# Performance work log

Measured on AMD Instinct MI355X. Metric: run time of the kernel, lower is better.

The kernel has to match this reference:

```python
import jax, jax.numpy as jnp
import numpy as np

G = 2048   # geneNum
E = 512    # emb_len
B = 16     # batch


def setup_inputs() -> dict:
    key = jax.random.key(0)
    ks = jax.random.split(key, 12)
    xav = 1.0 / np.sqrt(2.0)  # xavier gain used in reset_parameters

    def xavier(k, shape, gain):
        fan_in, fan_out = shape[1], shape[0]
        a = gain * np.sqrt(6.0 / (fan_in + fan_out))
        return jax.random.uniform(k, shape, jnp.float32, -a, a)

    return {
        "datax": jax.random.randint(ks[0], (B, G), 0, 5),
        "embMat": jax.random.normal(ks[1], (G, E), jnp.float32),      # frozen embedding table
        "Wq": xavier(ks[2], (E, E), xav),
        "Wk": xavier(ks[3], (E, E), xav),
        "k1": jax.random.normal(ks[4], (G, G), jnp.float32),
        "k2": jax.random.normal(ks[5], (G, G), jnp.float32),
        "k3": jax.random.normal(ks[6], (1,), jnp.float32),
        "shortestPath": jax.random.randint(ks[7], (G, G), 1, 8).astype(jnp.float32),
        "centralityMat": jax.random.uniform(ks[8], (G, G), jnp.float32),
        "padding": (jax.random.uniform(ks[9], (G, G)) > 0.1).astype(jnp.float32),
        "fc1_w": xavier(ks[10], (G, G), xav),
        "fc1_b": jnp.zeros((G,), jnp.float32),
        "fcCox_w": xavier(ks[11], (1, G), xav),
    }


def reference(datax, embMat, Wq, Wk, k1, k2, k3, shortestPath,
              centralityMat, padding, fc1_w, fc1_b, fcCox_w):
    # In torch, originalx aliases x, so the in-place binarization makes the
    # embedding indices binary (0/1).
    xbin = (datax != 0).astype(jnp.int32)          # [B, G]
    originalx = xbin.astype(jnp.float32)           # [B, G]
    x = embMat[xbin]                               # [B, G, E] (rows 0/1 of table)

    q = jnp.einsum('bge,fe->bgf', x, Wq)           # Linear no-bias: x @ Wq.T
    k = jnp.einsum('bge,fe->bgf', x, Wk)

    attn_weights = jnp.einsum('bge,bhe->bgh', q, k)  # [B, G, G]
    lrelu = lambda t: jax.nn.leaky_relu(t, 0.01)
    bias = (lrelu(k1) * shortestPath
            + lrelu(k2) * centralityMat
            + lrelu(k3) * padding)                 # [G, G]
    attn_weights = attn_weights + bias
    attn_weights_origin = attn_weights

    aw = jax.nn.softmax(attn_weights, axis=-1)     # [B, G, G]
    v = (datax != 0).astype(jnp.float32)           # binary values, [B, G]
    attn = jnp.einsum('bgh,bh->bg', aw, v)         # bmm with [B,G,1] + squeeze
    # Dropout(p=0.2) -> identity (eval / deterministic baseline)
    attn = originalx + attn
    attn = attn @ fc1_w.T + fc1_b                  # fc1
    output = attn @ fcCox_w.T                      # [B, 1]
    return output.reshape(-1), attn_weights_origin
```

## Files before the change

### kernel.cpp

```cpp
#include <hip/hip_runtime.h>
#include <stdint.h>

#define GN 2048
#define EN 512
#define BN 16

typedef unsigned int nt_u32x4 __attribute__((ext_vector_type(4)));
typedef float        nt_f32x4 __attribute__((ext_vector_type(4)));

__device__ __forceinline__ float bf2f(unsigned short u) {
    return __uint_as_float(((unsigned int)u) << 16);
}
__device__ __forceinline__ unsigned short f2bf(float f) {
    unsigned int u = __float_as_uint(f);
    u += 0x7fffu + ((u >> 16) & 1u);
    return (unsigned short)(u >> 16);
}
__device__ __forceinline__ float lrelu(float v) { return v > 0.f ? v : 0.01f * v; }

union U16x8 { uint4 v; nt_u32x4 e; unsigned short s[8]; };

template<bool ISBF>
__device__ __forceinline__ float ldf(const void* p, size_t i) {
    if (ISBF) return bf2f(((const unsigned short*)p)[i]);
    return ((const float*)p)[i];
}

template<bool ISBF>
__device__ __forceinline__ void ld8(const void* p, size_t off, float* v) {
    if (ISBF) {
        U16x8 u; u.v = *(const uint4*)((const unsigned short*)p + off);
        #pragma unroll
        for (int i = 0; i < 8; i++) v[i] = bf2f(u.s[i]);
    } else {
        const float* q = (const float*)p + off;
        const float4 a = *(const float4*)q;
        const float4 b = *(const float4*)(q + 4);
        v[0]=a.x; v[1]=a.y; v[2]=a.z; v[3]=a.w;
        v[4]=b.x; v[5]=b.y; v[6]=b.z; v[7]=b.w;
    }
}

template<bool ISBF>
__device__ __forceinline__ void st8(void* p, size_t off, const float* v) {
    if (ISBF) {
        U16x8 u;
        #pragma unroll
        for (int i = 0; i < 8; i++) u.s[i] = f2bf(v[i]);
        *(uint4*)((unsigned short*)p + off) = u.v;
    } else {
        float* q = (float*)p + off;
        *(float4*)q       = make_float4(v[0], v[1], v[2], v[3]);
        *(float4*)(q + 4) = make_float4(v[4], v[5], v[6], v[7]);
    }
}

__global__ void sniff_k(const unsigned int* __restrict__ emb, int* __restrict__ flag) {
    const int t = threadIdx.x;
    const unsigned int w = emb[t];
    const int e = (w >> 7) & 0xFF;
    const int ok = (e >= 108 && e <= 134) ? 1 : 0;
    const unsigned long long m = __ballot(ok);
    if (t == 0) flag[0] = (__popcll(m) >= 40) ? 1 : 0;
}

template<bool ISBF>
__device__ __forceinline__ void setup_body(
    const int* __restrict__ datax, const void* emb, const void* Wq, const void* Wk,
    const void* fc1w, const void* fcCox,
    unsigned char* __restrict__ xpackT, float* __restrict__ qk,
    float* __restrict__ partials)
{
    const int blk = blockIdx.x;
    const int t = threadIdx.x;

    if (blk < 16) {
        const int b = blk;
        unsigned int byte = 0;
        const int base = b * GN + t * 8;
        #pragma unroll
        for (int i = 0; i < 8; i++)
            byte |= (datax[base + i] != 0 ? 1u : 0u) << i;
        xpackT[t * 16 + b] = (unsigned char)byte;
    } else if (blk < 272) {
        const int iw = (blk - 16) * 4 + (t >> 6);
        const int lane = t & 63;
        const void* W = (iw < 512) ? Wq : Wk;
        const int f = iw & 511;
        float w8[8], e0[8], e1[8];
        ld8<ISBF>(W, (size_t)f * EN + lane * 8, w8);
        ld8<ISBF>(emb, (size_t)lane * 8, e0);
        ld8<ISBF>(emb, (size_t)EN + lane * 8, e1);
        float d0 = 0.f, d1 = 0.f;
        #pragma unroll
        for (int i = 0; i < 8; i++) { d0 += w8[i] * e0[i]; d1 += w8[i] * e1[i]; }
        for (int o = 32; o >= 1; o >>= 1) {
            d0 += __shfl_xor(d0, o);
            d1 += __shfl_xor(d1, o);
        }
        if (lane == 0) {
            const int base = (iw < 512) ? 0 : 1024;
            qk[base + f] = d0;
            qk[base + 512 + f] = d1;
        }
    } else {
        const int pb = blk - 272;
        float acc[8] = {0.f,0.f,0.f,0.f,0.f,0.f,0.f,0.f};
        for (int r = 0; r < 16; r++) {
            const int g = pb * 16 + r;
            const float c = ldf<ISBF>(fcCox, g);
            float w8[8];
            ld8<ISBF>(fc1w, (size_t)g * GN + t * 8, w8);
            #pragma unroll
            for (int i = 0; i < 8; i++) acc[i] += c * w8[i];
        }
        float* q = partials + (size_t)pb * GN + t * 8;
        *(float4*)q       = make_float4(acc[0], acc[1], acc[2], acc[3]);
        *(float4*)(q + 4) = make_float4(acc[4], acc[5], acc[6], acc[7]);
    }
}

__global__ __launch_bounds__(256) void setup_k(
    const int* datax, const void* emb, const void* Wq, const void* Wk,
    const void* fc1w, const void* fcCox,
    unsigned char* xpackT, float* qk, float* partials, const int* flag)
{
    if (flag[0]) setup_body<true>(datax, emb, Wq, Wk, fc1w, fcCox, xpackT, qk, partials);
    else         setup_body<false>(datax, emb, Wq, Wk, fc1w, fcCox, xpackT, qk, partials);
}

template<bool ISBF>
__device__ __forceinline__ void pre2_body(
    const float* __restrict__ qk, const void* fc1b, const void* fcCox,
    const float* __restrict__ partials,
    float* __restrict__ sv, float* __restrict__ cptr, float* __restrict__ weff)
{
    const int t = threadIdx.x;
    if (blockIdx.x > 0) {
        const int c = (blockIdx.x - 1) * 256 + t;
        float acc = 0.f;
        for (int r = 0; r < 128; r++)
            acc += partials[(size_t)r * GN + c];
        weff[c] = acc;
        return;
    }
    float a[5] = {0.f, 0.f, 0.f, 0.f, 0.f};
    for (int e = t; e < EN; e += 256) {
        float q0 = qk[e], q1 = qk[EN + e];
        float K0 = qk[2 * EN + e], K1 = qk[3 * EN + e];
        a[0] += q0 * K0; a[1] += q0 * K1; a[2] += q1 * K0; a[3] += q1 * K1;
    }
    for (int gg = t; gg < GN; gg += 256)
        a[4] += ldf<ISBF>(fc1b, gg) * ldf<ISBF>(fcCox, gg);
    for (int o = 32; o >= 1; o >>= 1)
        #pragma unroll
        for (int j = 0; j < 5; j++) a[j] += __shfl_xor(a[j], o);
    __shared__ float red[4][5];
    int wid = t >> 6, lane = t & 63;
    if (lane == 0)
        for (int j = 0; j < 5; j++) red[wid][j] = a[j];
    __syncthreads();
    if (t == 0) {
        for (int j = 0; j < 4; j++)
            sv[j] = red[0][j] + red[1][j] + red[2][j] + red[3][j];
        cptr[0] = red[0][4] + red[1][4] + red[2][4] + red[3][4];
    }
}

__global__ __launch_bounds__(256) void pre2_k(
    const float* qk, const void* fc1b, const void* fcCox, const float* partials,
    float* sv, float* cptr, float* weff, const int* flag)
{
    if (flag[0]) pre2_body<true>(qk, fc1b, fcCox, partials, sv, cptr, weff);
    else         pre2_body<false>(qk, fc1b, fcCox, partials, sv, cptr, weff);
}

template<bool ISBF>
__device__ __forceinline__ void attn_body(
    const void* k1, const void* k2, const void* k3,
    const void* sp, const void* cen, const void* pad,
    const unsigned char* __restrict__ xpackT, const float* __restrict__ sv,
    float* __restrict__ attn2, void* d_out)
{
    const int g = blockIdx.x;
    const int t = threadIdx.x;
    const int h0 = t << 3;
    const size_t roff = (size_t)g * GN + h0;

    const float lr3 = lrelu(ldf<ISBF>(k3, 0));

    float a1[8], a2[8], vsp[8], vcn[8], vpd[8];
    ld8<ISBF>(k1, roff, a1);
    ld8<ISBF>(k2, roff, a2);
    ld8<ISBF>(sp, roff, vsp);
    ld8<ISBF>(cen, roff, vcn);
    ld8<ISBF>(pad, roff, vpd);

    float bias8[8];
    float lmax = -3.4e38f;
    #pragma unroll
    for (int i = 0; i < 8; i++) {
        float b = lrelu(a1[i]) * vsp[i] + lrelu(a2[i]) * vcn[i] + lr3 * vpd[i];
        bias8[i] = b;
        lmax = fmaxf(lmax, b);
    }
    for (int o = 32; o >= 1; o >>= 1) lmax = fmaxf(lmax, __shfl_xor(lmax, o));

    __shared__ float smax[4];
    __shared__ float redT[4];
    __shared__ float red[4][BN];
    const int wid = t >> 6, lane = t & 63;
    if (lane == 0) smax[wid] = lmax;
    __syncthreads();
    const float Mg = fmaxf(fmaxf(smax[0], smax[1]), fmaxf(smax[2], smax[3]));

    float E8[8];
    float Tl = 0.f;
    #pragma unroll
    for (int i = 0; i < 8; i++) { E8[i] = __expf(bias8[i] - Mg); Tl += E8[i]; }

    const uint4 pk = *(const uint4*)(xpackT + (size_t)t * 16);
    const unsigned char* pb = (const unsigned char*)&pk;

    float s1l[BN];
    #pragma unroll
    for (int b = 0; b < BN; b++) {
        const unsigned int mk = pb[b];
        float acc1 = 0.f;
        #pragma unroll
        for (int i = 0; i < 8; i++)
            acc1 += ((mk >> i) & 1u) ? E8[i] : 0.f;
        s1l[b] = acc1;
    }
    for (int o = 32; o >= 1; o >>= 1) {
        Tl += __shfl_xor(Tl, o);
        #pragma unroll
        for (int b = 0; b < BN; b++) s1l[b] += __shfl_xor(s1l[b], o);
    }
    if (lane == 0) {
        redT[wid] = Tl;
        #pragma unroll
        for (int b = 0; b < BN; b++) red[wid][b] = s1l[b];
    }
    __syncthreads();

    const float s00 = sv[0], s01 = sv[1], s10 = sv[2], s11 = sv[3];
    const uint4 gk = *(const uint4*)(xpackT + (size_t)(g >> 3) * 16);
    const unsigned char* gb = (const unsigned char*)&gk;
    const int gbit = g & 7;

    if (t < BN) {
        const int b = t;
        const float Tg = redT[0] + redT[1] + redT[2] + redT[3];
        const float S1 = fmaxf(red[0][b] + red[1][b] + red[2][b] + red[3][b], 1e-30f);
        const float S0 = fmaxf(Tg - S1, 1e-30f);
        const bool on = ((gb[b] >> gbit) & 1u) != 0u;
        const float sa0 = on ? s10 : s00;
        const float sa1 = on ? s11 : s01;
        const float d = (sa0 + __logf(S0)) - (sa1 + __logf(S1));
        const float attnv = 1.f / (1.f + __expf(d));
        attn2[b * GN + g] = (on ? 1.f : 0.f) + attnv;
    }

    if (ISBF) {
        U16x8 p00, p01, p10, p11;
        #pragma unroll
        for (int i = 0; i < 8; i++) {
            p00.s[i] = f2bf(bias8[i] + s00);
            p01.s[i] = f2bf(bias8[i] + s01);
            p10.s[i] = f2bf(bias8[i] + s10);
            p11.s[i] = f2bf(bias8[i] + s11);
        }
        unsigned short* outp = (unsigned short*)d_out + BN + (size_t)g * GN + h0;
        #pragma unroll
        for (int b = 0; b < BN; b++) {
            const unsigned int mk = pb[b];
            const bool on = ((gb[b] >> gbit) & 1u) != 0u;
            U16x8 lo, hi;
            if (on) { lo = p10; hi = p11; } else { lo = p00; hi = p01; }
            U16x8 o;
            #pragma unroll
            for (int i = 0; i < 8; i++)
                o.s[i] = ((mk >> i) & 1u) ? hi.s[i] : lo.s[i];
            __builtin_nontemporal_store(o.e, (nt_u32x4*)(outp + (size_t)b * GN * GN));
        }
    } else {
        float v00[8], v01[8], v10[8], v11[8];
        #pragma unroll
        for (int i = 0; i < 8; i++) {
            v00[i] = bias8[i] + s00;
            v01[i] = bias8[i] + s01;
            v10[i] = bias8[i] + s10;
            v11[i] = bias8[i] + s11;
        }
        float* outp = (float*)d_out + BN + (size_t)g * GN + h0;
        #pragma unroll
        for (int b = 0; b < BN; b++) {
            const unsigned int mk = pb[b];
            const bool on = ((gb[b] >> gbit) & 1u) != 0u;
            float ov[8];
            #pragma unroll
            for (int i = 0; i < 8; i++) {
                const float lo = on ? v10[i] : v00[i];
                const float hi = on ? v11[i] : v01[i];
                ov[i] = ((mk >> i) & 1u) ? hi : lo;
            }
            float* q = outp + (size_t)b * GN * GN;
            nt_f32x4 lo4 = {ov[0], ov[1], ov[2], ov[3]};
            nt_f32x4 hi4 = {ov[4], ov[5], ov[6], ov[7]};
            __builtin_nontemporal_store(lo4, (nt_f32x4*)q);
            __builtin_nontemporal_store(hi4, (nt_f32x4*)(q + 4));
        }
    }
}

__global__ __launch_bounds__(256) void attn_k(
    const void* k1, const void* k2, const void* k3,
    const void* sp, const void* cen, const void* pad,
    const unsigned char* xpackT, const float* sv, float* attn2,
    void* d_out, const int* flag)
{
    if (flag[0]) attn_body<true>(k1, k2, k3, sp, cen, pad, xpackT, sv, attn2, d_out);
    else         attn_body<false>(k1, k2, k3, sp, cen, pad, xpackT, sv, attn2, d_out);
}

template<bool ISBF>
__device__ __forceinline__ void final_body(
    const float* __restrict__ attn2, const float* __restrict__ weff,
    const float* __restrict__ cptr, void* d_out)
{
    const int b = blockIdx.x, t = threadIdx.x;
    const int h0 = t << 3;
    const float4 a0 = *(const float4*)(attn2 + b * GN + h0);
    const float4 a1 = *(const float4*)(attn2 + b * GN + h0 + 4);
    const float4 w0 = *(const float4*)(weff + h0);
    const float4 w1 = *(const float4*)(weff + h0 + 4);
    float acc = a0.x * w0.x + a0.y * w0.y + a0.z * w0.z + a0.w * w0.w
              + a1.x * w1.x + a1.y * w1.y + a1.z * w1.z + a1.w * w1.w;
    for (int o = 32; o >= 1; o >>= 1) acc += __shfl_xor(acc, o);
    __shared__ float red[4];
    const int wid = t >> 6, lane = t & 63;
    if (lane == 0) red[wid] = acc;
    __syncthreads();
    if (t == 0) {
        const float val = cptr[0] + red[0] + red[1] + red[2] + red[3];
        if (ISBF) ((unsigned short*)d_out)[b] = f2bf(val);
        else      ((float*)d_out)[b] = val;
    }
}

__global__ __launch_bounds__(256) void final_k(
    const float* attn2, const float* weff, const float* cptr,
    void* d_out, const int* flag)
{
    if (flag[0]) final_body<true>(attn2, weff, cptr, d_out);
    else         final_body<false>(attn2, weff, cptr, d_out);
}

extern "C" void kernel_launch(void* const* d_in, const int* in_sizes, int n_in,
                              void* d_out, int out_size, void* d_ws, size_t ws_size,
                              hipStream_t stream) {
    const int*  datax = (const int*)d_in[0];
    const void* emb   = d_in[1];
    const void* Wq    = d_in[2];
    const void* Wk    = d_in[3];
    const void* k1    = d_in[4];
    const void* k2    = d_in[5];
    const void* k3    = d_in[6];
    const void* sp    = d_in[7];
    const void* cen   = d_in[8];
    const void* pad   = d_in[9];
    const void* fc1w  = d_in[10];
    const void* fc1b  = d_in[11];
    const void* fcCox = d_in[12];

    float* ws       = (float*)d_ws;
    float* qk       = ws;
    float* sv       = ws + 2048;
    float* cptr     = ws + 2052;
    float* weff     = ws + 2056;
    float* attn2    = ws + 4104;
    float* partials = ws + 36872;
    unsigned char* xpackT = (unsigned char*)(ws + 299016);
    int*   flag     = (int*)(ws + 300040);

    sniff_k<<<1, 64, 0, stream>>>((const unsigned int*)emb, flag);
    setup_k<<<400, 256, 0, stream>>>(datax, emb, Wq, Wk, fc1w, fcCox,
                                     xpackT, qk, partials, flag);
    pre2_k<<<9, 256, 0, stream>>>(qk, fc1b, fcCox, partials, sv, cptr, weff, flag);
    attn_k<<<GN, 256, 0, stream>>>(k1, k2, k3, sp, cen, pad, xpackT, sv, attn2, d_out, flag);
    final_k<<<BN, 256, 0, stream>>>(attn2, weff, cptr, d_out, flag);
}
```

Before: 454.2 us.

## Split attention kernel into bias/softmax pass and batch-wise output writer

The fused attention kernel is split into two kernels. The first computes the bias matrix once, writes it to a workspace buffer and does the softmax reductions. The second reads the bias back and writes the 16 batch slices, with each block covering one batch and 16 rows so writes are contiguous per batch. Nontemporal stores are also replaced with plain stores. This adds a 16 MB bias write and reread, plus an extra launch, in exchange for a different output write pattern. It depends on workspace size and falls back to the old kernel otherwise.

After: 515.4 us. 13.5% more time.

```diff
diff --git a/kernel.cpp b/kernel.cpp
--- a/kernel.cpp
+++ b/kernel.cpp
@@ -4,9 +4,6 @@
 #define GN 2048
 #define EN 512
 #define BN 16
-
-typedef unsigned int nt_u32x4 __attribute__((ext_vector_type(4)));
-typedef float        nt_f32x4 __attribute__((ext_vector_type(4)));
 
 __device__ __forceinline__ float bf2f(unsigned short u) {
     return __uint_as_float(((unsigned int)u) << 16);
@@ -18,7 +15,7 @@
 }
 __device__ __forceinline__ float lrelu(float v) { return v > 0.f ? v : 0.01f * v; }
 
-union U16x8 { uint4 v; nt_u32x4 e; unsigned short s[8]; };
+union U16x8 { uint4 v; unsigned short s[8]; };
 
 template<bool ISBF>
 __device__ __forceinline__ float ldf(const void* p, size_t i) {
@@ -38,20 +35,6 @@
         const float4 b = *(const float4*)(q + 4);
         v[0]=a.x; v[1]=a.y; v[2]=a.z; v[3]=a.w;
         v[4]=b.x; v[5]=b.y; v[6]=b.z; v[7]=b.w;
-    }
-}
-
-template<bool ISBF>
-__device__ __forceinline__ void st8(void* p, size_t off, const float* v) {
-    if (ISBF) {
-        U16x8 u;
-        #pragma unroll
-        for (int i = 0; i < 8; i++) u.s[i] = f2bf(v[i]);
-        *(uint4*)((unsigned short*)p + off) = u.v;
-    } else {
-        float* q = (float*)p + off;
-        *(float4*)q       = make_float4(v[0], v[1], v[2], v[3]);
-        *(float4*)(q + 4) = make_float4(v[4], v[5], v[6], v[7]);
     }
 }
 
@@ -176,6 +159,160 @@
 }
 
 template<bool ISBF>
+__device__ __forceinline__ void attnA_body(
+    const void* k1, const void* k2, const void* k3,
+    const void* sp, const void* cen, const void* pad,
+    const unsigned char* __restrict__ xpackT, const float* __restrict__ sv,
+    float* __restrict__ attn2, float* __restrict__ biasws)
+{
+    const int g = blockIdx.x;
+    const int t = threadIdx.x;
+    const int h0 = t << 3;
+    const size_t roff = (size_t)g * GN + h0;
+
+    const float lr3 = lrelu(ldf<ISBF>(k3, 0));
+
+    float a1[8], a2[8], vsp[8], vcn[8], vpd[8];
+    ld8<ISBF>(k1, roff, a1);
+    ld8<ISBF>(k2, roff, a2);
+    ld8<ISBF>(sp, roff, vsp);
+    ld8<ISBF>(cen, roff, vcn);
+    ld8<ISBF>(pad, roff, vpd);
+
+    float bias8[8];
+    float lmax = -3.4e38f;
+    #pragma unroll
+    for (int i = 0; i < 8; i++) {
+        float b = lrelu(a1[i]) * vsp[i] + lrelu(a2[i]) * vcn[i] + lr3 * vpd[i];
+        bias8[i] = b;
+        lmax = fmaxf(lmax, b);
+    }
+    float* bq = biasws + roff;
+    *(float4*)bq       = make_float4(bias8[0], bias8[1], bias8[2], bias8[3]);
+    *(float4*)(bq + 4) = make_float4(bias8[4], bias8[5], bias8[6], bias8[7]);
+
+    for (int o = 32; o >= 1; o >>= 1) lmax = fmaxf(lmax, __shfl_xor(lmax, o));
+
+    __shared__ float smax[4];
+    __shared__ float redT[4];
+    __shared__ float red[4][BN];
+    const int wid = t >> 6, lane = t & 63;
+    if (lane == 0) smax[wid] = lmax;
+    __syncthreads();
+    const float Mg = fmaxf(fmaxf(smax[0], smax[1]), fmaxf(smax[2], smax[3]));
+
+    float E8[8];
+    float Tl = 0.f;
+    #pragma unroll
+    for (int i = 0; i < 8; i++) { E8[i] = __expf(bias8[i] - Mg); Tl += E8[i]; }
+
+    const uint4 pk = *(const uint4*)(xpackT + (size_t)t * 16);
+    const unsigned char* pb = (const unsigned char*)&pk;
+
+    float s1l[BN];
+    #pragma unroll
+    for (int b = 0; b < BN; b++) {
+        const unsigned int mk = pb[b];
+        float acc1 = 0.f;
+        #pragma unroll
+        for (int i = 0; i < 8; i++)
+            acc1 += ((mk >> i) & 1u) ? E8[i] : 0.f;
+        s1l[b] = acc1;
+    }
+    for (int o = 32; o >= 1; o >>= 1) {
+        Tl += __shfl_xor(Tl, o);
+        #pragma unroll
+        for (int b = 0; b < BN; b++) s1l[b] += __shfl_xor(s1l[b], o);
+    }
+    if (lane == 0) {
+        redT[wid] = Tl;
+        #pragma unroll
+        for (int b = 0; b < BN; b++) red[wid][b] = s1l[b];
+    }
+    __syncthreads();
+
+    if (t < BN) {
+        const int b = t;
+        const float s00 = sv[0], s01 = sv[1], s10 = sv[2], s11 = sv[3];
+        const uint4 gk = *(const uint4*)(xpackT + (size_t)(g >> 3) * 16);
+        const unsigned char* gb = (const unsigned char*)&gk;
+        const int gbit = g & 7;
+        const float Tg = redT[0] + redT[1] + redT[2] + redT[3];
+        const float S1 = fmaxf(red[0][b] + red[1][b] + red[2][b] + red[3][b], 1e-30f);
+        const float S0 = fmaxf(Tg - S1, 1e-30f);
+        const bool on = ((gb[b] >> gbit) & 1u) != 0u;
+        const float sa0 = on ? s10 : s00;
+        const float sa1 = on ? s11 : s01;
+        const float d = (sa0 + __logf(S0)) - (sa1 + __logf(S1));
+        const float attnv = 1.f / (1.f + __expf(d));
+        attn2[b * GN + g] = (on ? 1.f : 0.f) + attnv;
+    }
+}
+
+__global__ __launch_bounds__(256) void attnA_k(
+    const void* k1, const void* k2, const void* k3,
+    const void* sp, const void* cen, const void* pad,
+    const unsigned char* xpackT, const float* sv, float* attn2,
+    float* biasws, const int* flag)
+{
+    if (flag[0]) attnA_body<true>(k1, k2, k3, sp, cen, pad, xpackT, sv, attn2, biasws);
+    else         attnA_body<false>(k1, k2, k3, sp, cen, pad, xpackT, sv, attn2, biasws);
+}
+
+template<bool ISBF>
+__device__ __forceinline__ void attnB_body(
+    const float* __restrict__ biasws, const unsigned char* __restrict__ xpackT,
+    const float* __restrict__ sv, void* d_out)
+{
+    const int id = blockIdx.x;
+    const int b  = id & 15;
+    const int ch = id >> 4;
+    const int t  = threadIdx.x;
+    const int h0 = t << 3;
+
+    const float s00 = sv[0], s01 = sv[1], s10 = sv[2], s11 = sv[3];
+    const unsigned int mk = xpackT[t * 16 + b];
+
+    #pragma unroll 2
+    for (int r = 0; r < 16; r++) {
+        const int g = ch * 16 + r;
+        const unsigned int gbyte = xpackT[(g >> 3) * 16 + b];
+        const bool on = ((gbyte >> (g & 7)) & 1u) != 0u;
+        const float c0 = on ? s10 : s00;
+        const float c1 = on ? s11 : s01;
+
+        const float* br = biasws + (size_t)g * GN + h0;
+        const float4 x0 = *(const float4*)br;
+        const float4 x1 = *(const float4*)(br + 4);
+        float v[8] = {x0.x, x0.y, x0.z, x0.w, x1.x, x1.y, x1.z, x1.w};
+        float ov[8];
+        #pragma unroll
+        for (int i = 0; i < 8; i++)
+            ov[i] = v[i] + (((mk >> i) & 1u) ? c1 : c0);
+
+        const size_t ooff = (size_t)b * GN * GN + (size_t)g * GN + h0;
+        if (ISBF) {
+            U16x8 u;
+            #pragma unroll
+            for (int i = 0; i < 8; i++) u.s[i] = f2bf(ov[i]);
+            *(uint4*)((unsigned short*)d_out + BN + ooff) = u.v;
+        } else {
+            float* q = (float*)d_out + BN + ooff;
+            *(float4*)q       = make_float4(ov[0], ov[1], ov[2], ov[3]);
+            *(float4*)(q + 4) = make_float4(ov[4], ov[5], ov[6], ov[7]);
+        }
+    }
+}
+
+__global__ __launch_bounds__(256) void attnB_k(
+    const float* biasws, const unsigned char* xpackT, const float* sv,
+    void* d_out, const int* flag)
+{
+    if (flag[0]) attnB_body<true>(biasws, xpackT, sv, d_out);
+    else         attnB_body<false>(biasws, xpackT, sv, d_out);
+}
+
+template<bool ISBF>
 __device__ __forceinline__ void attn_body(
     const void* k1, const void* k2, const void* k3,
     const void* sp, const void* cen, const void* pad,
@@ -282,7 +419,7 @@
             #pragma unroll
             for (int i = 0; i < 8; i++)
                 o.s[i] = ((mk >> i) & 1u) ? hi.s[i] : lo.s[i];
-            __builtin_nontemporal_store(o.e, (nt_u32x4*)(outp + (size_t)b * GN * GN));
+            *(uint4*)(outp + (size_t)b * GN * GN) = o.v;
         }
     } else {
         float v00[8], v01[8], v10[8], v11[8];
@@ -306,10 +443,8 @@
                 ov[i] = ((mk >> i) & 1u) ? hi : lo;
             }
             float* q = outp + (size_t)b * GN * GN;
-            nt_f32x4 lo4 = {ov[0], ov[1], ov[2], ov[3]};
-            nt_f32x4 hi4 = {ov[4], ov[5], ov[6], ov[7]};
-            __builtin_nontemporal_store(lo4, (nt_f32x4*)q);
-            __builtin_nontemporal_store(hi4, (nt_f32x4*)(q + 4));
+            *(float4*)q       = make_float4(ov[0], ov[1], ov[2], ov[3]);
+            *(float4*)(q + 4) = make_float4(ov[4], ov[5], ov[6], ov[7]);
         }
     }
 }
@@ -383,11 +518,21 @@
     float* partials = ws + 36872;
     unsigned char* xpackT = (unsigned char*)(ws + 299016);
     int*   flag     = (int*)(ws + 300040);
+    const size_t WS_BIAS_OFF = 302080;
+    float* biasws   = ws + WS_BIAS_OFF;
+    const size_t WS_NEED = (WS_BIAS_OFF + (size_t)GN * GN) * sizeof(float);
 
     sniff_k<<<1, 64, 0, stream>>>((const unsigned int*)emb, flag);
     setup_k<<<400, 256, 0, stream>>>(datax, emb, Wq, Wk, fc1w, fcCox,
                                      xpackT, qk, partials, flag);
     pre2_k<<<9, 256, 0, stream>>>(qk, fc1b, fcCox, partials, sv, cptr, weff, flag);
-    attn_k<<<GN, 256, 0, stream>>>(k1, k2, k3, sp, cen, pad, xpackT, sv, attn2, d_out, flag);
+    if (ws_size >= WS_NEED) {
+        attnA_k<<<GN, 256, 0, stream>>>(k1, k2, k3, sp, cen, pad, xpackT, sv,
+                                        attn2, biasws, flag);
+        attnB_k<<<GN, 256, 0, stream>>>(biasws, xpackT, sv, d_out, flag);
+    } else {
+        attn_k<<<GN, 256, 0, stream>>>(k1, k2, k3, sp, cen, pad, xpackT, sv,
+                                       attn2, d_out, flag);
+    }
     final_k<<<BN, 256, 0, stream>>>(attn2, weff, cptr, d_out, flag);
 }
```
